# Performance work log

Measured on AMD Instinct MI355X. Metric: run time of the kernel, lower is better.

The kernel has to match this reference:

```python
import jax, jax.numpy as jnp
import numpy as np

NE, NR = 100000, 50
E, H, M = 512, 8, 8
HD = E // H
B = 65536


def setup_inputs() -> dict:
    key = jax.random.key(0)
    ks = jax.random.split(key, 24)
    xav = lambda k, shp: jax.random.normal(k, shp, jnp.float32) * (2.0 / (shp[0] + shp[-1])) ** 0.5
    return {
        'entity_emb': xav(ks[0], (NE, E)),
        'relation_emb': xav(ks[1], (NR, E)),
        'dens_ent_emb': jax.random.normal(ks[2], (NE, E), jnp.float32) * 0.02,
        'dens_ent_w': xav(ks[3], (E, 1)), 'dens_ent_b': jnp.zeros((1,), jnp.float32),
        'dens_rel_emb': jax.random.normal(ks[4], (NR, E), jnp.float32) * 0.02,
        'dens_rel_w': xav(ks[5], (E, 1)), 'dens_rel_b': jnp.zeros((1,), jnp.float32),
        'local_motifs': xav(ks[6], (M, HD)),
        'global_motifs': xav(ks[7], (M, HD)),
        'Wq': xav(ks[8], (E, E)), 'bq': jnp.zeros((E,), jnp.float32),
        'Wkl': xav(ks[9], (HD, HD)), 'bkl': jnp.zeros((HD,), jnp.float32),
        'Wkg': xav(ks[10], (HD, HD)), 'bkg': jnp.zeros((HD,), jnp.float32),
        'Wout': xav(ks[11], (2 * E, E)), 'bout': jnp.zeros((E,), jnp.float32),
        'adv_w': jnp.float32(1.0), 'adv_b': jnp.float32(0.0),
        'h_idx': jax.random.randint(ks[12], (B,), 0, NE),
        'r_idx': jax.random.randint(ks[13], (B,), 0, NR),
        't_idx': jax.random.randint(ks[14], (B,), 0, NE),
    }


def reference(entity_emb, relation_emb, dens_ent_emb, dens_ent_w, dens_ent_b,
              dens_rel_emb, dens_rel_w, dens_rel_b, local_motifs, global_motifs,
              Wq, bq, Wkl, bkl, Wkg, bkg, Wout, bout, adv_w, adv_b,
              h_idx, r_idx, t_idx):
    h = entity_emb[h_idx]           # [B, E]
    r = relation_emb[r_idx]
    t = entity_emb[t_idx]
    # density gating: sigmoid(Linear(Embedding(idx))) per head/tail/relation, averaged
    h_d = jax.nn.sigmoid(dens_ent_emb[h_idx] @ dens_ent_w + dens_ent_b)   # [B,1]
    t_d = jax.nn.sigmoid(dens_ent_emb[t_idx] @ dens_ent_w + dens_ent_b)
    r_d = jax.nn.sigmoid(dens_rel_emb[r_idx] @ dens_rel_w + dens_rel_b)
    density = (h_d + t_d + r_d) / 3.0                                     # [B,1]
    diff = h + r - t
    # hierarchical soft attention over local/global motif codebooks
    ctx = h + r + t
    q = (ctx @ Wq + bq).reshape(-1, H, HD)                                # [B,H,HD]
    lk = local_motifs @ Wkl + bkl                                         # [M,HD]
    gk = global_motifs @ Wkg + bkg
    scale = 1.0 / jnp.sqrt(jnp.asarray(HD, q.dtype))
    dens = density[:, :, None]                                            # [B,1,1]
    l_w = jax.nn.softmax(jnp.einsum('bhd,md->bhm', q, lk) * scale + dens, axis=-1)
    g_w = jax.nn.softmax(jnp.einsum('bhd,md->bhm', q, gk) * scale + dens, axis=-1)
    attn = (l_w + g_w) / 2.0                                              # [B,H,M]
    motifs = local_motifs + global_motifs                                 # [M,HD]
    motif_repr = jnp.einsum('bhm,md->bhd', attn, motifs).reshape(-1, E)   # [B,E]
    motif_loss = jnp.sum((diff - motif_repr) ** 2, axis=-1)               # ||.||^2
    combined = jnp.concatenate([diff, motif_repr], axis=-1)               # [B,2E]
    transformed = jnp.tanh(combined @ Wout + bout)
    score = adv_w * jnp.linalg.norm(transformed, axis=-1) + adv_b
    return score, motif_loss
```

## Files before the change

### kernel.cpp

```cpp
#include <hip/hip_runtime.h>
#include <math.h>

#define B_TOT 65536

typedef __attribute__((ext_vector_type(4))) float f32x4;
typedef __attribute__((ext_vector_type(4))) unsigned int u32x4;
typedef __attribute__((ext_vector_type(8))) __bf16 bf16x8;

#define OFF_WLOGT 0u
#define OFF_CBIAS 131072u
#define OFF_BCAT  131584u
#define OFF_MOTIF 721408u
#define OFF_LK    723456u
#define OFF_GK    725504u
#define OFF_G     727552u
#define OFF_DIFF  1048576u
#define OFF_ATTN  68157440u

__device__ __forceinline__ unsigned short f2bf(float x) {
  union { float f; unsigned int u; } v; v.f = x;
  return (unsigned short)((v.u + 0x7FFFu + ((v.u >> 16) & 1u)) >> 16);
}

__device__ __forceinline__ float bf2f(unsigned short u) {
  union { unsigned int i; float f; } v; v.i = ((unsigned int)u) << 16; return v.f;
}

__global__ __launch_bounds__(256) void k0a(
    const float* __restrict__ lm, const float* __restrict__ gm,
    const float* __restrict__ Wkl, const float* __restrict__ bkl,
    const float* __restrict__ Wkg, const float* __restrict__ bkg,
    const float* __restrict__ bq,
    float* __restrict__ lk, float* __restrict__ gk,
    float* __restrict__ motifs, float* __restrict__ G, float* __restrict__ cb) {
  int tid = threadIdx.x;
  for (int o = tid; o < 512; o += 256) {
    int m = o >> 6, d = o & 63;
    float s1 = bkl[d], s2 = bkg[d];
    for (int k = 0; k < 64; ++k) {
      s1 += lm[m*64+k] * Wkl[k*64+d];
      s2 += gm[m*64+k] * Wkg[k*64+d];
    }
    lk[o] = s1; gk[o] = s2;
    motifs[o] = lm[o] + gm[o];
  }
  __syncthreads();
  if (tid < 64) {
    int m = tid >> 3, n = tid & 7;
    float s = 0.f;
    for (int d = 0; d < 64; ++d) s += motifs[m*64+d] * motifs[n*64+d];
    G[tid] = s;
  }
  if (tid < 128) {
    int s_ = tid >> 6, h = (tid >> 3) & 7, m = tid & 7;
    const float* K = s_ ? gk : lk;
    float s = 0.f;
    for (int d = 0; d < 64; ++d) s += bq[h*64+d] * K[m*64+d];
    cb[tid] = 0.125f * s;
  }
}

__global__ __launch_bounds__(256) void k0b(
    const float* __restrict__ Wq, const float* __restrict__ Wout,
    const float* __restrict__ lk, const float* __restrict__ gk,
    const float* __restrict__ motifs,
    unsigned short* __restrict__ wlogT, unsigned short* __restrict__ bcatT) {
  int idx = blockIdx.x * 256 + threadIdx.x;
  if (idx >= 65536 + 512*576) return;
  if (idx < 65536) {
    int c = idx >> 9, k = idx & 511;
    int s_ = c >> 6, h = (c >> 3) & 7, m = c & 7;
    const float* K = (s_ ? gk : lk) + m*64;
    const float* wq = Wq + (size_t)k*512 + h*64;
    float s = 0.f;
    for (int d = 0; d < 64; ++d) s += wq[d] * K[d];
    wlogT[(size_t)c*512 + k] = f2bf(0.125f * s);
  } else {
    int i2 = idx - 65536;
    int n = i2 / 576, k = i2 - n*576;
    float v;
    if (k < 512) {
      v = Wout[(size_t)k*512 + n];
    } else {
      int hm = k - 512, h = hm >> 3, m = hm & 7;
      const float* mo = motifs + m*64;
      const float* wo = Wout + (size_t)(512 + h*64)*512 + n;
      v = 0.f;
      for (int d = 0; d < 64; ++d) v += mo[d] * wo[(size_t)d*512];
    }
    bcatT[(size_t)n*576 + k] = f2bf(v);
  }
}

__global__ __launch_bounds__(256, 3) void kA(
    const float* __restrict__ ent, const float* __restrict__ rel,
    const int* __restrict__ hI, const int* __restrict__ rI, const int* __restrict__ tI,
    const unsigned short* __restrict__ wlogT, const float* __restrict__ cb,
    unsigned short* __restrict__ diffB, unsigned short* __restrict__ attnB) {
  __shared__ __align__(16) unsigned char smem[32768];
  unsigned short* As = (unsigned short*)smem;
  unsigned short* Bs = (unsigned short*)(smem + 9216);
  float* lg  = (float*)smem;

  int tid = threadIdx.x;
  int l = tid & 63, wid = tid >> 6;
  int wr = wid >> 1, wc = wid & 1;
  int rowBase = blockIdx.x * 64;
  int r_loc = tid >> 2, p = tid & 3;
  int b = rowBase + r_loc;

  int hi = hI[b], ri = rI[b], ti = tI[b];
  const float* hp = ent + (size_t)hi * 512;
  const float* tp = ent + (size_t)ti * 512;
  const float* rp = rel + (size_t)ri * 512;
  int bn = tid >> 1, half = tid & 1;
  const unsigned short* wsrc = wlogT + (size_t)bn * 512 + half * 32;

  f32x4 acc[2][4] = {};

  float4 gh[4], gt[4], gr[4];
  u32x4 wb[4];

  {
    int q0 = p*8, q1 = 32 + p*8;
    gh[0] = *(const float4*)(hp + q0); gh[1] = *(const float4*)(hp + q0 + 4);
    gh[2] = *(const float4*)(hp + q1); gh[3] = *(const float4*)(hp + q1 + 4);
    gt[0] = *(const float4*)(tp + q0); gt[1] = *(const float4*)(tp + q0 + 4);
    gt[2] = *(const float4*)(tp + q1); gt[3] = *(const float4*)(tp + q1 + 4);
    gr[0] = *(const float4*)(rp + q0); gr[1] = *(const float4*)(rp + q0 + 4);
    gr[2] = *(const float4*)(rp + q1); gr[3] = *(const float4*)(rp + q1 + 4);
    #pragma unroll
    for (int o = 0; o < 4; ++o) wb[o] = *(const u32x4*)(wsrc + o*8);
  }

  #pragma unroll
  for (int c = 0; c < 8; ++c) {
    int k0 = c * 64;
    float df[16], cx[16];
    #pragma unroll
    for (int g = 0; g < 4; ++g) {
      #pragma unroll
      for (int j = 0; j < 4; ++j) {
        float hv = ((const float*)&gh[g])[j];
        float tv = ((const float*)&gt[g])[j];
        float rv = ((const float*)&gr[g])[j];
        df[g*4+j] = hv + rv - tv;
        cx[g*4+j] = hv + rv + tv;
      }
    }
    union { u32x4 v[2]; unsigned short s[16]; } pd, pc;
    #pragma unroll
    for (int j = 0; j < 16; ++j) { pd.s[j] = f2bf(df[j]); pc.s[j] = f2bf(cx[j]); }

    __syncthreads();
    *(u32x4*)(As + r_loc*72 + p*8)      = pc.v[0];
    *(u32x4*)(As + r_loc*72 + 32 + p*8) = pc.v[1];
    {
      unsigned short* bp = Bs + bn*72 + half*32;
      *(u32x4*)(bp)      = wb[0];
      *(u32x4*)(bp + 8)  = wb[1];
      *(u32x4*)(bp + 16) = wb[2];
      *(u32x4*)(bp + 24) = wb[3];
    }
    *(u32x4*)(diffB + (size_t)b*512 + k0 + p*8)      = pd.v[0];
    *(u32x4*)(diffB + (size_t)b*512 + k0 + 32 + p*8) = pd.v[1];
    __syncthreads();
    if (c < 7) {
      int q0 = k0 + 64 + p*8, q1 = k0 + 96 + p*8;
      gh[0] = *(const float4*)(hp + q0); gh[1] = *(const float4*)(hp + q0 + 4);
      gh[2] = *(const float4*)(hp + q1); gh[3] = *(const float4*)(hp + q1 + 4);
      gt[0] = *(const float4*)(tp + q0); gt[1] = *(const float4*)(tp + q0 + 4);
      gt[2] = *(const float4*)(tp + q1); gt[3] = *(const float4*)(tp + q1 + 4);
      gr[0] = *(const float4*)(rp + q0); gr[1] = *(const float4*)(rp + q0 + 4);
      gr[2] = *(const float4*)(rp + q1); gr[3] = *(const float4*)(rp + q1 + 4);
      #pragma unroll
      for (int o = 0; o < 4; ++o) wb[o] = *(const u32x4*)(wsrc + (c+1)*64 + o*8);
    }
    #pragma unroll
    for (int kf = 0; kf < 2; ++kf) {
      bf16x8 af0 = *(const bf16x8*)(As + (wr*32 +      (l & 15))*72 + kf*32 + 8*(l >> 4));
      bf16x8 af1 = *(const bf16x8*)(As + (wr*32 + 16 + (l & 15))*72 + kf*32 + 8*(l >> 4));
      #pragma unroll
      for (int n = 0; n < 4; ++n) {
        bf16x8 bfr = *(const bf16x8*)(Bs + (wc*64 + n*16 + (l & 15))*72 + kf*32 + 8*(l >> 4));
        acc[0][n] = __builtin_amdgcn_mfma_f32_16x16x32_bf16(af0, bfr, acc[0][n], 0, 0, 0);
        acc[1][n] = __builtin_amdgcn_mfma_f32_16x16x32_bf16(af1, bfr, acc[1][n], 0, 0, 0);
      }
    }
  }

  __syncthreads();
  #pragma unroll
  for (int m = 0; m < 2; ++m)
    #pragma unroll
    for (int n = 0; n < 4; ++n)
      #pragma unroll
      for (int j = 0; j < 4; ++j) {
        int rr = wr*32 + m*16 + 4*(l >> 4) + j;
        int cc = wc*64 + n*16 + (l & 15);
        lg[rr*128 + ((cc + rr) & 127)] = acc[m][n][j];
      }
  __syncthreads();

  #pragma unroll
  for (int e = 0; e < 2; ++e) {
    int h = 2*p + e;
    float a8[8];
    #pragma unroll
    for (int m = 0; m < 8; ++m) a8[m] = 0.f;
    #pragma unroll
    for (int s = 0; s < 2; ++s) {
      float v[8], mx = -1e30f;
      #pragma unroll
      for (int m = 0; m < 8; ++m) {
        int cc = s*64 + h*8 + m;
        v[m] = lg[r_loc*128 + ((cc + r_loc) & 127)] + cb[cc];
        mx = fmaxf(mx, v[m]);
      }
      float sum = 0.f;
      #pragma unroll
      for (int m = 0; m < 8; ++m) { v[m] = __expf(v[m] - mx); sum += v[m]; }
      float inv = 0.5f / sum;
      #pragma unroll
      for (int m = 0; m < 8; ++m) a8[m] += v[m] * inv;
    }
    union { u32x4 v; unsigned short s[8]; } pk;
    #pragma unroll
    for (int m = 0; m < 8; ++m) pk.s[m] = f2bf(a8[m]);
    *(u32x4*)(attnB + (size_t)b*64 + h*8) = pk.v;
  }
}

__global__ __launch_bounds__(256) void kC(
    const unsigned short* __restrict__ diffB, const unsigned short* __restrict__ attnB,
    const float* __restrict__ motifs, float* __restrict__ lossOut) {
  __shared__ float mo[512];
  int tid = threadIdx.x;
  mo[tid] = motifs[tid];
  mo[tid + 256] = motifs[tid + 256];
  __syncthreads();
  int l = tid & 63;
  int b = blockIdx.x * 4 + (tid >> 6);
  union { u32x4 v; unsigned short s[8]; } dv, av;
  dv.v = *(const u32x4*)(diffB + (size_t)b*512 + l*8);
  int h = l >> 3;
  av.v = *(const u32x4*)(attnB + (size_t)b*64 + h*8);
  float at[8], df[8];
  #pragma unroll
  for (int j = 0; j < 8; ++j) { df[j] = bf2f(dv.s[j]); at[j] = bf2f(av.s[j]); }
  int dbase = (l & 7) * 8;
  float part = 0.f;
  #pragma unroll
  for (int j = 0; j < 8; ++j) {
    float repr = 0.f;
    #pragma unroll
    for (int m = 0; m < 8; ++m) repr += at[m] * mo[m*64 + dbase + j];
    float e = df[j] - repr;
    part += e * e;
  }
  #pragma unroll
  for (int off = 1; off < 64; off <<= 1) part += __shfl_xor(part, off, 64);
  if (l == 0) lossOut[b] = part;
}

__global__ __launch_bounds__(512, 2) void kB(
    const unsigned short* __restrict__ diffB, const unsigned short* __restrict__ attnB,
    const unsigned short* __restrict__ bcatT, const float* __restrict__ bout,
    const float* __restrict__ advw, const float* __restrict__ advb,
    float* __restrict__ scoreOut) {
  __shared__ __align__(16) unsigned short As[2][128*40];
  __shared__ __align__(16) unsigned short Bs[2][512*40];
  __shared__ float part[128*4];
  int tid = threadIdx.x;
  int l = tid & 63, wid = tid >> 6;
  int wr = wid >> 2, wc = wid & 3;
  int rowBase = blockIdx.x * 128;
  f32x4 acc[4][8] = {};
  int ar = tid >> 2, aq = tid & 3;
  int bn = tid, bx = (bn >> 3) & 3;

  u32x4 va;
  u32x4 vb[4];
  {
    va = *(const u32x4*)(diffB + (size_t)(rowBase + ar)*512 + aq*8);
    const u32x4* src = (const u32x4*)(bcatT + (size_t)bn*576);
    vb[0] = src[0]; vb[1] = src[1]; vb[2] = src[2]; vb[3] = src[3];
    *(u32x4*)(&As[0][ar*40 + aq*8]) = va;
    unsigned short* bp = &Bs[0][bn*40];
    *(u32x4*)(bp + (0^bx)*8) = vb[0];
    *(u32x4*)(bp + (1^bx)*8) = vb[1];
    *(u32x4*)(bp + (2^bx)*8) = vb[2];
    *(u32x4*)(bp + (3^bx)*8) = vb[3];
  }
  int cur = 0;
  for (int ks = 0; ks < 18; ++ks) {
    __syncthreads();
    u32x4 na; u32x4 nb[4];
    if (ks < 17) {
      int k0 = (ks + 1) * 32;
      const unsigned short* srcp = (k0 < 512)
        ? diffB + (size_t)(rowBase + ar)*512 + k0 + aq*8
        : attnB + (size_t)(rowBase + ar)*64 + (k0 - 512) + aq*8;
      na = *(const u32x4*)srcp;
      const u32x4* src = (const u32x4*)(bcatT + (size_t)bn*576 + k0);
      nb[0] = src[0]; nb[1] = src[1]; nb[2] = src[2]; nb[3] = src[3];
    }
    {
      bf16x8 af[4];
      #pragma unroll
      for (int m = 0; m < 4; ++m)
        af[m] = *(const bf16x8*)(&As[cur][(wr*64 + m*16 + (l & 15))*40 + 8*(l >> 4)]);
      #pragma unroll
      for (int n = 0; n < 8; ++n) {
        int col = wc*128 + n*16 + (l & 15);
        int g = (l >> 4) ^ ((col >> 3) & 3);
        bf16x8 bfr = *(const bf16x8*)(&Bs[cur][col*40 + g*8]);
        #pragma unroll
        for (int m = 0; m < 4; ++m)
          acc[m][n] = __builtin_amdgcn_mfma_f32_16x16x32_bf16(af[m], bfr, acc[m][n], 0, 0, 0);
      }
    }
    if (ks < 17) {
      *(u32x4*)(&As[cur^1][ar*40 + aq*8]) = na;
      unsigned short* bp = &Bs[cur^1][bn*40];
      *(u32x4*)(bp + (0^bx)*8) = nb[0];
      *(u32x4*)(bp + (1^bx)*8) = nb[1];
      *(u32x4*)(bp + (2^bx)*8) = nb[2];
      *(u32x4*)(bp + (3^bx)*8) = nb[3];
    }
    cur ^= 1;
  }
  __syncthreads();
  float aw = advw[0], ab = advb[0];
  float bo[8];
  #pragma unroll
  for (int n = 0; n < 8; ++n) bo[n] = bout[wc*128 + n*16 + (l & 15)];
  #pragma unroll
  for (int m = 0; m < 4; ++m) {
    float ss0 = 0.f, ss1 = 0.f, ss2 = 0.f, ss3 = 0.f;
    #pragma unroll
    for (int n = 0; n < 8; ++n) {
      float t0 = tanhf(acc[m][n][0] + bo[n]); ss0 += t0*t0;
      float t1 = tanhf(acc[m][n][1] + bo[n]); ss1 += t1*t1;
      float t2 = tanhf(acc[m][n][2] + bo[n]); ss2 += t2*t2;
      float t3 = tanhf(acc[m][n][3] + bo[n]); ss3 += t3*t3;
    }
    #pragma unroll
    for (int mask = 1; mask < 16; mask <<= 1) {
      ss0 += __shfl_xor(ss0, mask, 64);
      ss1 += __shfl_xor(ss1, mask, 64);
      ss2 += __shfl_xor(ss2, mask, 64);
      ss3 += __shfl_xor(ss3, mask, 64);
    }
    if ((l & 15) == 0) {
      int rbase = wr*64 + m*16 + (l >> 4)*4;
      part[(rbase+0)*4 + wc] = ss0;
      part[(rbase+1)*4 + wc] = ss1;
      part[(rbase+2)*4 + wc] = ss2;
      part[(rbase+3)*4 + wc] = ss3;
    }
  }
  __syncthreads();
  if (tid < 128) {
    float s = part[tid*4] + part[tid*4+1] + part[tid*4+2] + part[tid*4+3];
    scoreOut[rowBase + tid] = aw * sqrtf(s) + ab;
  }
}

extern "C" void kernel_launch(void* const* d_in, const int* in_sizes, int n_in,
                              void* d_out, int out_size, void* d_ws, size_t ws_size,
                              hipStream_t stream) {
  const float* ent  = (const float*)d_in[0];
  const float* rel  = (const float*)d_in[1];
  const float* lm   = (const float*)d_in[8];
  const float* gm   = (const float*)d_in[9];
  const float* Wq   = (const float*)d_in[10];
  const float* bq   = (const float*)d_in[11];
  const float* Wkl  = (const float*)d_in[12];
  const float* bkl  = (const float*)d_in[13];
  const float* Wkg  = (const float*)d_in[14];
  const float* bkg  = (const float*)d_in[15];
  const float* Wout = (const float*)d_in[16];
  const float* bout = (const float*)d_in[17];
  const float* advw = (const float*)d_in[18];
  const float* advb = (const float*)d_in[19];
  const int* hI = (const int*)d_in[20];
  const int* rI = (const int*)d_in[21];
  const int* tI = (const int*)d_in[22];
  char* ws = (char*)d_ws;
  unsigned short* wlogT = (unsigned short*)(ws + OFF_WLOGT);
  float* cb     = (float*)(ws + OFF_CBIAS);
  unsigned short* bcatT = (unsigned short*)(ws + OFF_BCAT);
  float* motifs = (float*)(ws + OFF_MOTIF);
  float* lk     = (float*)(ws + OFF_LK);
  float* gk     = (float*)(ws + OFF_GK);
  float* G      = (float*)(ws + OFF_G);
  unsigned short* diffB = (unsigned short*)(ws + OFF_DIFF);
  unsigned short* attnB = (unsigned short*)(ws + OFF_ATTN);
  float* scoreOut = (float*)d_out;
  float* lossOut  = (float*)d_out + B_TOT;

  hipLaunchKernelGGL(k0a, dim3(1), dim3(256), 0, stream,
                     lm, gm, Wkl, bkl, Wkg, bkg, bq, lk, gk, motifs, G, cb);
  hipLaunchKernelGGL(k0b, dim3(1408), dim3(256), 0, stream,
                     Wq, Wout, lk, gk, motifs, wlogT, bcatT);
  hipLaunchKernelGGL(kA, dim3(B_TOT/64), dim3(256), 0, stream,
                     ent, rel, hI, rI, tI, wlogT, cb, diffB, attnB);
  hipLaunchKernelGGL(kC, dim3(B_TOT/4), dim3(256), 0, stream,
                     diffB, attnB, motifs, lossOut);
  hipLaunchKernelGGL(kB, dim3(B_TOT/128), dim3(512), 0, stream,
                     diffB, attnB, bcatT, bout, advw, advb, scoreOut);
}
```

Before: 181.0 us.

## Merge motif-loss kernel into output GEMM launch and raise kA occupancy hint

Folds the separate loss kernel kC into the kB launch as extra blocks appended to the grid. Each extra block computes the loss for 128 rows, with four threads per row and a short shuffle reduction, reusing the part shared buffer for the motifs. This removes one kernel launch and lets the loss work overlap with the GEMM blocks. It also raises kA's launch_bounds minimum from 3 to 4 blocks and converts to bf16 in place rather than through float temporaries, which may cap registers and cause spills.

```diff
diff --git a/kernel.cpp b/kernel.cpp
--- a/kernel.cpp
+++ b/kernel.cpp
@@ -92,7 +92,7 @@
   }
 }
 
-__global__ __launch_bounds__(256, 3) void kA(
+__global__ __launch_bounds__(256, 4) void kA(
     const float* __restrict__ ent, const float* __restrict__ rel,
     const int* __restrict__ hI, const int* __restrict__ rI, const int* __restrict__ tI,
     const unsigned short* __restrict__ wlogT, const float* __restrict__ cb,
@@ -136,7 +136,7 @@
   #pragma unroll
   for (int c = 0; c < 8; ++c) {
     int k0 = c * 64;
-    float df[16], cx[16];
+    union { u32x4 v[2]; unsigned short s[16]; } pd, pc;
     #pragma unroll
     for (int g = 0; g < 4; ++g) {
       #pragma unroll
@@ -144,13 +144,10 @@
         float hv = ((const float*)&gh[g])[j];
         float tv = ((const float*)&gt[g])[j];
         float rv = ((const float*)&gr[g])[j];
-        df[g*4+j] = hv + rv - tv;
-        cx[g*4+j] = hv + rv + tv;
-      }
-    }
-    union { u32x4 v[2]; unsigned short s[16]; } pd, pc;
-    #pragma unroll
-    for (int j = 0; j < 16; ++j) { pd.s[j] = f2bf(df[j]); pc.s[j] = f2bf(cx[j]); }
+        pd.s[g*4+j] = f2bf(hv + rv - tv);
+        pc.s[g*4+j] = f2bf(hv + rv + tv);
+      }
+    }
 
     __syncthreads();
     *(u32x4*)(As + r_loc*72 + p*8)      = pc.v[0];
@@ -231,47 +228,52 @@
   }
 }
 
-__global__ __launch_bounds__(256) void kC(
-    const unsigned short* __restrict__ diffB, const unsigned short* __restrict__ attnB,
-    const float* __restrict__ motifs, float* __restrict__ lossOut) {
-  __shared__ float mo[512];
-  int tid = threadIdx.x;
-  mo[tid] = motifs[tid];
-  mo[tid + 256] = motifs[tid + 256];
-  __syncthreads();
-  int l = tid & 63;
-  int b = blockIdx.x * 4 + (tid >> 6);
-  union { u32x4 v; unsigned short s[8]; } dv, av;
-  dv.v = *(const u32x4*)(diffB + (size_t)b*512 + l*8);
-  int h = l >> 3;
-  av.v = *(const u32x4*)(attnB + (size_t)b*64 + h*8);
-  float at[8], df[8];
-  #pragma unroll
-  for (int j = 0; j < 8; ++j) { df[j] = bf2f(dv.s[j]); at[j] = bf2f(av.s[j]); }
-  int dbase = (l & 7) * 8;
-  float part = 0.f;
-  #pragma unroll
-  for (int j = 0; j < 8; ++j) {
-    float repr = 0.f;
-    #pragma unroll
-    for (int m = 0; m < 8; ++m) repr += at[m] * mo[m*64 + dbase + j];
-    float e = df[j] - repr;
-    part += e * e;
-  }
-  #pragma unroll
-  for (int off = 1; off < 64; off <<= 1) part += __shfl_xor(part, off, 64);
-  if (l == 0) lossOut[b] = part;
-}
-
-__global__ __launch_bounds__(512, 2) void kB(
+__global__ __launch_bounds__(512, 2) void kBC(
     const unsigned short* __restrict__ diffB, const unsigned short* __restrict__ attnB,
     const unsigned short* __restrict__ bcatT, const float* __restrict__ bout,
     const float* __restrict__ advw, const float* __restrict__ advb,
-    float* __restrict__ scoreOut) {
+    const float* __restrict__ motifs,
+    float* __restrict__ scoreOut, float* __restrict__ lossOut) {
   __shared__ __align__(16) unsigned short As[2][128*40];
   __shared__ __align__(16) unsigned short Bs[2][512*40];
   __shared__ float part[128*4];
   int tid = threadIdx.x;
+
+  if (blockIdx.x >= B_TOT/128) {
+    int blk = blockIdx.x - B_TOT/128;
+    part[tid] = motifs[tid];
+    __syncthreads();
+    int row = blk*128 + (tid >> 2), aq = tid & 3;
+    const unsigned short* dp = diffB + (size_t)row*512 + aq*128;
+    const unsigned short* ap = attnB + (size_t)row*64 + aq*16;
+    union { u32x4 v; unsigned short s[8]; } au0, au1;
+    au0.v = *(const u32x4*)(ap);
+    au1.v = *(const u32x4*)(ap + 8);
+    float at[2][8];
+    #pragma unroll
+    for (int m = 0; m < 8; ++m) { at[0][m] = bf2f(au0.s[m]); at[1][m] = bf2f(au1.s[m]); }
+    float lp = 0.f;
+    #pragma unroll
+    for (int c = 0; c < 16; ++c) {
+      union { u32x4 v; unsigned short s[8]; } du;
+      du.v = *(const u32x4*)(dp + c*8);
+      int hsel = c >> 3;
+      int dbase = (c & 7) * 8;
+      #pragma unroll
+      for (int j = 0; j < 8; ++j) {
+        float repr = 0.f;
+        #pragma unroll
+        for (int m = 0; m < 8; ++m) repr += at[hsel][m] * part[m*64 + dbase + j];
+        float e = bf2f(du.s[j]) - repr;
+        lp += e * e;
+      }
+    }
+    lp += __shfl_xor(lp, 1, 64);
+    lp += __shfl_xor(lp, 2, 64);
+    if (aq == 0) lossOut[row] = lp;
+    return;
+  }
+
   int l = tid & 63, wid = tid >> 6;
   int wr = wid >> 2, wc = wid & 3;
   int rowBase = blockIdx.x * 128;
@@ -406,8 +408,6 @@
                      Wq, Wout, lk, gk, motifs, wlogT, bcatT);
   hipLaunchKernelGGL(kA, dim3(B_TOT/64), dim3(256), 0, stream,
                      ent, rel, hI, rI, tI, wlogT, cb, diffB, attnB);
-  hipLaunchKernelGGL(kC, dim3(B_TOT/4), dim3(256), 0, stream,
-                     diffB, attnB, motifs, lossOut);
-  hipLaunchKernelGGL(kB, dim3(B_TOT/128), dim3(512), 0, stream,
-                     diffB, attnB, bcatT, bout, advw, advb, scoreOut);
-}
+  hipLaunchKernelGGL(kBC, dim3(B_TOT/128 + B_TOT/128), dim3(512), 0, stream,
+                     diffB, attnB, bcatT, bout, advw, advb, motifs, scoreOut, lossOut);
+}
```

After: 237.9 us. 1.31x slower.

## Single-buffer kB shared memory and raise occupancy bounds for kA and kB

Applied to the files above, without the earlier changes.

kB drops its double-buffered LDS tiles for one buffer, which costs an extra barrier per k-step, and raises launch bounds to 4 blocks per CU. kA's launch bound also goes to 4 blocks, and its bf16 packing is fused directly into the add loop. The aim is to fit more waves per CU to hide gather and global-load latency. The risk is register spilling in kB: it holds 128 accumulator floats per thread and would be capped at a lower register budget.

```diff
diff --git a/kernel.cpp b/kernel.cpp
--- a/kernel.cpp
+++ b/kernel.cpp
@@ -92,7 +92,7 @@
   }
 }
 
-__global__ __launch_bounds__(256, 3) void kA(
+__global__ __launch_bounds__(256, 4) void kA(
     const float* __restrict__ ent, const float* __restrict__ rel,
     const int* __restrict__ hI, const int* __restrict__ rI, const int* __restrict__ tI,
     const unsigned short* __restrict__ wlogT, const float* __restrict__ cb,
@@ -136,7 +136,7 @@
   #pragma unroll
   for (int c = 0; c < 8; ++c) {
     int k0 = c * 64;
-    float df[16], cx[16];
+    union { u32x4 v[2]; unsigned short s[16]; } pd, pc;
     #pragma unroll
     for (int g = 0; g < 4; ++g) {
       #pragma unroll
@@ -144,13 +144,10 @@
         float hv = ((const float*)&gh[g])[j];
         float tv = ((const float*)&gt[g])[j];
         float rv = ((const float*)&gr[g])[j];
-        df[g*4+j] = hv + rv - tv;
-        cx[g*4+j] = hv + rv + tv;
+        pd.s[g*4+j] = f2bf(hv + rv - tv);
+        pc.s[g*4+j] = f2bf(hv + rv + tv);
       }
     }
-    union { u32x4 v[2]; unsigned short s[16]; } pd, pc;
-    #pragma unroll
-    for (int j = 0; j < 16; ++j) { pd.s[j] = f2bf(df[j]); pc.s[j] = f2bf(cx[j]); }
 
     __syncthreads();
     *(u32x4*)(As + r_loc*72 + p*8)      = pc.v[0];
@@ -263,13 +260,13 @@
   if (l == 0) lossOut[b] = part;
 }
 
-__global__ __launch_bounds__(512, 2) void kB(
+__global__ __launch_bounds__(512, 4) void kB(
     const unsigned short* __restrict__ diffB, const unsigned short* __restrict__ attnB,
     const unsigned short* __restrict__ bcatT, const float* __restrict__ bout,
     const float* __restrict__ advw, const float* __restrict__ advb,
     float* __restrict__ scoreOut) {
-  __shared__ __align__(16) unsigned short As[2][128*40];
-  __shared__ __align__(16) unsigned short Bs[2][512*40];
+  __shared__ __align__(16) unsigned short As[128*40];
+  __shared__ __align__(16) unsigned short Bs[512*40];
   __shared__ float part[128*4];
   int tid = threadIdx.x;
   int l = tid & 63, wid = tid >> 6;
@@ -279,23 +276,24 @@
   int ar = tid >> 2, aq = tid & 3;
   int bn = tid, bx = (bn >> 3) & 3;
 
-  u32x4 va;
-  u32x4 vb[4];
+  u32x4 na;
+  u32x4 nb[4];
   {
-    va = *(const u32x4*)(diffB + (size_t)(rowBase + ar)*512 + aq*8);
+    na = *(const u32x4*)(diffB + (size_t)(rowBase + ar)*512 + aq*8);
     const u32x4* src = (const u32x4*)(bcatT + (size_t)bn*576);
-    vb[0] = src[0]; vb[1] = src[1]; vb[2] = src[2]; vb[3] = src[3];
-    *(u32x4*)(&As[0][ar*40 + aq*8]) = va;
-    unsigned short* bp = &Bs[0][bn*40];
-    *(u32x4*)(bp + (0^bx)*8) = vb[0];
-    *(u32x4*)(bp + (1^bx)*8) = vb[1];
-    *(u32x4*)(bp + (2^bx)*8) = vb[2];
-    *(u32x4*)(bp + (3^bx)*8) = vb[3];
-  }
-  int cur = 0;
+    nb[0] = src[0]; nb[1] = src[1]; nb[2] = src[2]; nb[3] = src[3];
+  }
   for (int ks = 0; ks < 18; ++ks) {
     __syncthreads();
-    u32x4 na; u32x4 nb[4];
+    *(u32x4*)(&As[ar*40 + aq*8]) = na;
+    {
+      unsigned short* bp = &Bs[bn*40];
+      *(u32x4*)(bp + (0^bx)*8) = nb[0];
+      *(u32x4*)(bp + (1^bx)*8) = nb[1];
+      *(u32x4*)(bp + (2^bx)*8) = nb[2];
+      *(u32x4*)(bp + (3^bx)*8) = nb[3];
+    }
+    __syncthreads();
     if (ks < 17) {
       int k0 = (ks + 1) * 32;
       const unsigned short* srcp = (k0 < 512)
@@ -309,26 +307,17 @@
       bf16x8 af[4];
       #pragma unroll
       for (int m = 0; m < 4; ++m)
-        af[m] = *(const bf16x8*)(&As[cur][(wr*64 + m*16 + (l & 15))*40 + 8*(l >> 4)]);
+        af[m] = *(const bf16x8*)(&As[(wr*64 + m*16 + (l & 15))*40 + 8*(l >> 4)]);
       #pragma unroll
       for (int n = 0; n < 8; ++n) {
         int col = wc*128 + n*16 + (l & 15);
         int g = (l >> 4) ^ ((col >> 3) & 3);
-        bf16x8 bfr = *(const bf16x8*)(&Bs[cur][col*40 + g*8]);
+        bf16x8 bfr = *(const bf16x8*)(&Bs[col*40 + g*8]);
         #pragma unroll
         for (int m = 0; m < 4; ++m)
           acc[m][n] = __builtin_amdgcn_mfma_f32_16x16x32_bf16(af[m], bfr, acc[m][n], 0, 0, 0);
       }
     }
-    if (ks < 17) {
-      *(u32x4*)(&As[cur^1][ar*40 + aq*8]) = na;
-      unsigned short* bp = &Bs[cur^1][bn*40];
-      *(u32x4*)(bp + (0^bx)*8) = nb[0];
-      *(u32x4*)(bp + (1^bx)*8) = nb[1];
-      *(u32x4*)(bp + (2^bx)*8) = nb[2];
-      *(u32x4*)(bp + (3^bx)*8) = nb[3];
-    }
-    cur ^= 1;
   }
   __syncthreads();
   float aw = advw[0], ab = advb[0];
```

Measured after the change: 392.2 us. 117% more time.
